# Optimization experiments

Measured on AMD Instinct MI355X. Metric: run time of the kernel, lower is better.

The kernel has to match this reference:

```python
import jax, jax.numpy as jnp
import numpy as np

N_NODES = 50000
N_EDGES = 800000
IN_F = 128
HID = 64
H1 = 4  # heads layer 1
H2 = 1  # heads layer 2
N_GRAPHS = 32
NEG_SLOPE = 0.2  # PyG GATConv default leaky_relu slope


def _glorot(key, shape):
    fan_in, fan_out = shape[0], shape[-1]
    scale = jnp.sqrt(6.0 / (fan_in + fan_out))
    return jax.random.uniform(key, shape, jnp.float32, -scale, scale)


def setup_inputs() -> dict:
    key = jax.random.key(0)
    ks = jax.random.split(key, 10)
    x = jax.random.normal(ks[0], (N_NODES, IN_F), jnp.float32)
    edge_index = jax.random.randint(ks[1], (2, N_EDGES), 0, N_NODES, jnp.int64)
    batch = jnp.sort(jax.random.randint(ks[2], (N_NODES,), 0, N_GRAPHS, jnp.int64))
    # GATConv layer 1: in 128 -> 4 heads x 64, concat
    W1 = _glorot(ks[3], (IN_F, H1 * HID))
    a_src1 = _glorot(ks[4], (H1, HID))
    a_dst1 = _glorot(ks[5], (H1, HID))
    b1 = jnp.zeros((H1 * HID,), jnp.float32)
    # GATConv layer 2: in 256 -> 1 head x 64
    W2 = _glorot(ks[6], (H1 * HID, H2 * HID))
    a_src2 = _glorot(ks[7], (H2, HID))
    a_dst2 = _glorot(ks[8], (H2, HID))
    b2 = jnp.zeros((H2 * HID,), jnp.float32)
    return {"x": x, "edge_index": edge_index, "batch": batch,
            "W1": W1, "a_src1": a_src1, "a_dst1": a_dst1, "b1": b1,
            "W2": W2, "a_src2": a_src2, "a_dst2": a_dst2, "b2": b2}


def gat_layer(x, src, dst, W, a_src, a_dst, bias, num_nodes):
    """PyG-style GATConv with concat=True output [N, H*C]."""
    H, C = a_src.shape
    h = (x @ W).reshape(num_nodes, H, C)            # [N,H,C]
    alpha_src = jnp.sum(h * a_src[None], axis=-1)   # [N,H]
    alpha_dst = jnp.sum(h * a_dst[None], axis=-1)   # [N,H]
    e = jax.nn.leaky_relu(alpha_src[src] + alpha_dst[dst], NEG_SLOPE)  # [E,H]
    # segment softmax over destination neighborhoods
    m = jax.ops.segment_max(e, dst, num_segments=num_nodes)
    ex = jnp.exp(e - m[dst])
    denom = jax.ops.segment_sum(ex, dst, num_segments=num_nodes)
    alpha = ex / (denom[dst] + 1e-16)               # [E,H]
    out = jax.ops.segment_sum(h[src] * alpha[:, :, None], dst, num_segments=num_nodes)
    return out.reshape(num_nodes, H * C) + bias


def reference(x, edge_index, batch, W1, a_src1, a_dst1, b1, W2, a_src2, a_dst2, b2):
    N = x.shape[0]
    # PyG GATConv adds self-loops by default
    loops = jnp.arange(N, dtype=edge_index.dtype)
    src = jnp.concatenate([edge_index[0], loops])
    dst = jnp.concatenate([edge_index[1], loops])
    h = jax.nn.relu(gat_layer(x, src, dst, W1, a_src1, a_dst1, b1, N))
    h = gat_layer(h, src, dst, W2, a_src2, a_dst2, b2, N)
    # role == 'global': global mean pool over batch ids
    sums = jax.ops.segment_sum(h, batch, num_segments=N_GRAPHS)
    cnt = jax.ops.segment_sum(jnp.ones((N, 1), h.dtype), batch, num_segments=N_GRAPHS)
    return sums / jnp.maximum(cnt, 1.0)
```

## Files before the change

### kernel.cpp

```cpp
#include <hip/hip_runtime.h>
#include <cmath>

#define HID 64
typedef unsigned short ushort_t;
typedef __attribute__((ext_vector_type(8))) short bf16x8;
typedef __attribute__((ext_vector_type(4))) float f32x4;

__device__ inline ushort_t f2b(float f) {
    unsigned u = __float_as_uint(f);
    unsigned r = (u + 0x7fffu + ((u >> 16) & 1u)) >> 16;
    return (ushort_t)r;
}
__device__ inline float b2f(ushort_t b) { return __uint_as_float(((unsigned)b) << 16); }


__global__ void fill_i32(int* __restrict__ p, int v, long n) {
    long i = (long)blockIdx.x * blockDim.x + threadIdx.x;
    long stride = (long)gridDim.x * blockDim.x;
    for (; i < n; i += stride) p[i] = v;
}

__global__ __launch_bounds__(256) void prep_k(const float* __restrict__ W1,
                                              const float* __restrict__ W2,
                                              ushort_t* __restrict__ W1t,
                                              ushort_t* __restrict__ W2t,
                                              const int* __restrict__ batch,
                                              int* __restrict__ cnt_i,
                                              float* __restrict__ outp,
                                              int N, int NHB) {
    int b = blockIdx.x;
    int t = threadIdx.x;
    if (b < 128) {
        W1t[(size_t)t * 128 + b] = f2b(W1[(size_t)b * 256 + t]);
    } else if (b < 384) {
        int k = b - 128;
        if (t < 64) W2t[(size_t)t * 256 + k] = f2b(W2[(size_t)k * 64 + t]);
    } else if (b < 384 + NHB) {
        __shared__ int lh[32];
        if (t < 32) lh[t] = 0;
        __syncthreads();
        int i = (b - 384) * 256 + t;
        if (i < N) atomicAdd(&lh[batch[i]], 1);
        __syncthreads();
        if (t < 32 && lh[t] > 0) atomicAdd(&cnt_i[t], lh[t]);
    } else {
        int i = t * 8;
        #pragma unroll
        for (int j = 0; j < 8; ++j) outp[i + j] = 0.f;
    }
}

template<int WM, int WN, int K, bool AF32, bool B_WHOLE, int AH>
__global__ __launch_bounds__(WM * WN * 64) void gemm_mfma(
        const void* __restrict__ Ap, const ushort_t* __restrict__ Bt,
        ushort_t* __restrict__ Cb, const float* __restrict__ a_src,
        const float* __restrict__ a_dst, float* __restrict__ os,
        float* __restrict__ od, int M) {
    constexpr int T = WM * WN * 64;
    constexpr int BM = WM * 64;
    constexpr int BN = WN * 64;
    constexpr int BSTR = B_WHOLE ? (K + 8) : 40;

    __shared__ ushort_t Alds[BM][40];
    __shared__ ushort_t Blds[BN][BSTR];

    const int tid = threadIdx.x;
    const int bm = blockIdx.x * BM;
    const int w = tid >> 6;
    const int l = tid & 63;
    const int lr = l >> 4;
    const int lc = l & 15;
    const int row0 = (WM == 1) ? 0 : w * 64;
    const int col0 = (WN == 1) ? 0 : w * 64;

    f32x4 acc[4][4] = {};

    if (B_WHOLE) {
        constexpr int UPR = K / 8;
        for (int u = tid; u < BN * UPR; u += T) {
            int row = u / UPR, j = u % UPR;
            *(bf16x8*)&Blds[row][j * 8] = *(const bf16x8*)&Bt[(size_t)row * K + j * 8];
        }
    }

    for (int kk = 0; kk < K / 32; ++kk) {
        __syncthreads();
        for (int u = tid; u < BM * 4; u += T) {
            int row = u >> 2, part = u & 3;
            int gm = bm + row;
            bf16x8 v = {0, 0, 0, 0, 0, 0, 0, 0};
            if (gm < M) {
                if (AF32) {
                    const float* ap = (const float*)Ap + (size_t)gm * K + kk * 32 + part * 8;
                    float4 v0 = *(const float4*)ap;
                    float4 v1 = *(const float4*)(ap + 4);
                    v[0] = (short)f2b(v0.x); v[1] = (short)f2b(v0.y);
                    v[2] = (short)f2b(v0.z); v[3] = (short)f2b(v0.w);
                    v[4] = (short)f2b(v1.x); v[5] = (short)f2b(v1.y);
                    v[6] = (short)f2b(v1.z); v[7] = (short)f2b(v1.w);
                } else {
                    v = *(const bf16x8*)((const ushort_t*)Ap + (size_t)gm * K + kk * 32 + part * 8);
                }
            }
            *(bf16x8*)&Alds[row][part * 8] = v;
        }
        if (!B_WHOLE) {
            for (int u = tid; u < BN * 4; u += T) {
                int col = u >> 2, part = u & 3;
                *(bf16x8*)&Blds[col][part * 8] =
                    *(const bf16x8*)&Bt[(size_t)col * K + kk * 32 + part * 8];
            }
        }
        __syncthreads();

        const int koff = B_WHOLE ? kk * 32 : 0;
        bf16x8 af[4], bfr[4];
        #pragma unroll
        for (int fr = 0; fr < 4; ++fr)
            af[fr] = *(const bf16x8*)&Alds[row0 + fr * 16 + lc][lr * 8];
        #pragma unroll
        for (int fc = 0; fc < 4; ++fc)
            bfr[fc] = *(const bf16x8*)&Blds[col0 + fc * 16 + lc][koff + lr * 8];
        #pragma unroll
        for (int fr = 0; fr < 4; ++fr)
            #pragma unroll
            for (int fc = 0; fc < 4; ++fc)
                acc[fr][fc] = __builtin_amdgcn_mfma_f32_16x16x32_bf16(
                    af[fr], bfr[fc], acc[fr][fc], 0, 0, 0);
    }

    #pragma unroll
    for (int fr = 0; fr < 4; ++fr)
        #pragma unroll
        for (int r = 0; r < 4; ++r) {
            int gm = bm + row0 + fr * 16 + lr * 4 + r;
            if (gm >= M) continue;
            #pragma unroll
            for (int fc = 0; fc < 4; ++fc)
                Cb[(size_t)gm * BN + col0 + fc * 16 + lc] = f2b(acc[fr][fc][r]);
        }

    if (AH > 0) {
        const int head = (WN > 1) ? w : 0;
        const float* __restrict__ asv = a_src + head * 64;
        const float* __restrict__ adv = a_dst + head * 64;
        #pragma unroll
        for (int fr = 0; fr < 4; ++fr)
            #pragma unroll
            for (int r = 0; r < 4; ++r) {
                float ps = 0.f, pd = 0.f;
                #pragma unroll
                for (int fc = 0; fc < 4; ++fc) {
                    float av = acc[fr][fc][r];
                    ps = fmaf(av, asv[fc * 16 + lc], ps);
                    pd = fmaf(av, adv[fc * 16 + lc], pd);
                }
                #pragma unroll
                for (int off = 1; off < 16; off <<= 1) {
                    ps += __shfl_xor(ps, off, 64);
                    pd += __shfl_xor(pd, off, 64);
                }
                int gm = bm + row0 + fr * 16 + lr * 4 + r;
                if (lc == 0 && gm < M) {
                    os[(size_t)gm * AH + head] = ps;
                    od[(size_t)gm * AH + head] = pd;
                }
            }
    }
}


__global__ void count_k(const int* __restrict__ ei, int E, int N, int* __restrict__ deg) {
    int e = blockIdx.x * blockDim.x + threadIdx.x;
    int T = E + N;
    if (e >= T) return;
    int d = (e < E) ? ei[E + e] : (e - E);
    atomicAdd(&deg[d], 1);
}

__global__ __launch_bounds__(256) void scan1_k(const int* __restrict__ deg,
                                               int* __restrict__ bsum, int N) {
    int i = blockIdx.x * 256 + threadIdx.x;
    int v = (i < N) ? deg[i] : 0;
    #pragma unroll
    for (int off = 32; off > 0; off >>= 1) v += __shfl_xor(v, off, 64);
    __shared__ int ws[4];
    if ((threadIdx.x & 63) == 0) ws[threadIdx.x >> 6] = v;
    __syncthreads();
    if (threadIdx.x == 0) bsum[blockIdx.x] = ws[0] + ws[1] + ws[2] + ws[3];
}

__global__ __launch_bounds__(256) void scan3_k(const int* __restrict__ deg,
                                               const int* __restrict__ bsum,
                                               int* __restrict__ rowstart, int N, int NB) {
    int t = threadIdx.x;
    int lane = t & 63, wave = t >> 6;
    int pv = (t < NB && t < (int)blockIdx.x) ? bsum[t] : 0;
    #pragma unroll
    for (int off = 32; off > 0; off >>= 1) pv += __shfl_xor(pv, off, 64);
    __shared__ int wsp[4];
    if (lane == 0) wsp[wave] = pv;
    __syncthreads();
    int base = wsp[0] + wsp[1] + wsp[2] + wsp[3];

    int i = blockIdx.x * 256 + t;
    int v = (i < N) ? deg[i] : 0;
    int inc = v;
    #pragma unroll
    for (int off = 1; off < 64; off <<= 1) {
        int u = __shfl_up(inc, off, 64);
        if (lane >= off) inc += u;
    }
    __shared__ int wsum[4];
    if (lane == 63) wsum[wave] = inc;
    __syncthreads();
    int woff = base;
    for (int w = 0; w < wave; ++w) woff += wsum[w];
    int excl = inc - v + woff;
    if (i < N) rowstart[i] = excl;
    if (i == N - 1) rowstart[N] = excl + v;
}

__global__ void scatter_k(const int* __restrict__ ei, int E, int N,
                          const int* __restrict__ rowstart, int* __restrict__ cursor,
                          int* __restrict__ srcs) {
    int e = blockIdx.x * blockDim.x + threadIdx.x;
    int T = E + N;
    if (e >= T) return;
    int s, d;
    if (e < E) { s = ei[e]; d = ei[E + e]; } else { s = e - E; d = s; }
    int p = atomicAdd(&cursor[d], 1);
    srcs[rowstart[d] + p] = s;
}

#define MAXD 128
__global__ __launch_bounds__(256) void gat_agg4(const ushort_t* __restrict__ hb,
        const int* __restrict__ rowstart, const int* __restrict__ srcs,
        const float* __restrict__ as, const float* __restrict__ ad,
        const float* __restrict__ bias, ushort_t* __restrict__ outb, int N) {
    __shared__ int ssrc_s[4][MAXD];
    __shared__ float sw_s[4][MAXD][4];
    __shared__ float hstat_s[4][2][4];
    const int wave = threadIdx.x >> 6;
    const int lane = threadIdx.x & 63;
    int d = blockIdx.x * 4 + wave;
    if (d >= N) return;
    int* ssrc = ssrc_s[wave];
    float (*sw)[4] = sw_s[wave];
    int beg = rowstart[d];
    int deg = rowstart[d + 1] - beg;
    int dcap = deg < MAXD ? deg : MAXD;
    for (int i = lane; i < dcap; i += 64) ssrc[i] = srcs[beg + i];

    const int isub = lane >> 2;
    const int hd = lane & 3;
    float adv = ad[d * 4 + hd];
    float vmax = -INFINITY;
    for (int e0 = 0; e0 < deg; e0 += 16) {
        int e = e0 + isub;
        if (e < deg) {
            int s = (e < MAXD) ? ssrc[e] : srcs[beg + e];
            float v = as[s * 4 + hd] + adv;
            v = v > 0.f ? v : 0.2f * v;
            if (e < MAXD) sw[e][hd] = v;
            vmax = fmaxf(vmax, v);
        }
    }
    #pragma unroll
    for (int off = 4; off < 64; off <<= 1) vmax = fmaxf(vmax, __shfl_xor(vmax, off, 64));
    float dsum = 0.f;
    for (int e0 = 0; e0 < deg; e0 += 16) {
        int e = e0 + isub;
        if (e < deg) {
            float v;
            if (e < MAXD) v = sw[e][hd];
            else {
                int s = srcs[beg + e];
                v = as[s * 4 + hd] + adv;
                v = v > 0.f ? v : 0.2f * v;
            }
            float ex = __expf(v - vmax);
            if (e < MAXD) sw[e][hd] = ex;
            dsum += ex;
        }
    }
    #pragma unroll
    for (int off = 4; off < 64; off <<= 1) dsum += __shfl_xor(dsum, off, 64);
    float rden = 1.f / (dsum + 1e-16f);
    for (int e0 = 0; e0 < dcap; e0 += 16) {
        int e = e0 + isub;
        if (e < dcap) sw[e][hd] *= rden;
    }
    if (deg > MAXD && isub == 0) {
        hstat_s[wave][0][hd] = vmax;
        hstat_s[wave][1][hd] = rden;
    }

    const int hd2 = lane >> 4;
    const ushort_t* __restrict__ hrow = hb + (size_t)(lane * 4);
    float a0 = 0.f, a1 = 0.f, a2 = 0.f, a3 = 0.f;
    int e = 0;
    for (; e + 4 <= dcap; e += 4) {
        int s0 = __builtin_amdgcn_readfirstlane(ssrc[e]);
        int s1 = __builtin_amdgcn_readfirstlane(ssrc[e + 1]);
        int s2 = __builtin_amdgcn_readfirstlane(ssrc[e + 2]);
        int s3 = __builtin_amdgcn_readfirstlane(ssrc[e + 3]);
        ushort4 g0 = *(const ushort4*)(hrow + (size_t)s0 * 256);
        ushort4 g1 = *(const ushort4*)(hrow + (size_t)s1 * 256);
        ushort4 g2 = *(const ushort4*)(hrow + (size_t)s2 * 256);
        ushort4 g3 = *(const ushort4*)(hrow + (size_t)s3 * 256);
        float w0 = sw[e][hd2], w1 = sw[e + 1][hd2];
        float w2 = sw[e + 2][hd2], w3 = sw[e + 3][hd2];
        a0 = fmaf(b2f(g0.x), w0, a0); a1 = fmaf(b2f(g0.y), w0, a1);
        a2 = fmaf(b2f(g0.z), w0, a2); a3 = fmaf(b2f(g0.w), w0, a3);
        a0 = fmaf(b2f(g1.x), w1, a0); a1 = fmaf(b2f(g1.y), w1, a1);
        a2 = fmaf(b2f(g1.z), w1, a2); a3 = fmaf(b2f(g1.w), w1, a3);
        a0 = fmaf(b2f(g2.x), w2, a0); a1 = fmaf(b2f(g2.y), w2, a1);
        a2 = fmaf(b2f(g2.z), w2, a2); a3 = fmaf(b2f(g2.w), w2, a3);
        a0 = fmaf(b2f(g3.x), w3, a0); a1 = fmaf(b2f(g3.y), w3, a1);
        a2 = fmaf(b2f(g3.z), w3, a2); a3 = fmaf(b2f(g3.w), w3, a3);
    }
    for (; e < dcap; ++e) {
        int s = __builtin_amdgcn_readfirstlane(ssrc[e]);
        float w = sw[e][hd2];
        ushort4 g = *(const ushort4*)(hrow + (size_t)s * 256);
        a0 = fmaf(b2f(g.x), w, a0); a1 = fmaf(b2f(g.y), w, a1);
        a2 = fmaf(b2f(g.z), w, a2); a3 = fmaf(b2f(g.w), w, a3);
    }
    if (deg > MAXD) {
        float vm2 = hstat_s[wave][0][hd2];
        float rd2 = hstat_s[wave][1][hd2];
        float adv2 = ad[d * 4 + hd2];
        for (int j = MAXD; j < deg; ++j) {
            int s = srcs[beg + j];
            float v = as[s * 4 + hd2] + adv2;
            v = v > 0.f ? v : 0.2f * v;
            float w = __expf(v - vm2) * rd2;
            ushort4 g = *(const ushort4*)(hrow + (size_t)s * 256);
            a0 = fmaf(b2f(g.x), w, a0); a1 = fmaf(b2f(g.y), w, a1);
            a2 = fmaf(b2f(g.z), w, a2); a3 = fmaf(b2f(g.w), w, a3);
        }
    }
    int cb = lane * 4;
    ushort4 ov;
    ov.x = f2b(fmaxf(a0 + bias[cb + 0], 0.f));
    ov.y = f2b(fmaxf(a1 + bias[cb + 1], 0.f));
    ov.z = f2b(fmaxf(a2 + bias[cb + 2], 0.f));
    ov.w = f2b(fmaxf(a3 + bias[cb + 3], 0.f));
    *(ushort4*)&outb[(size_t)d * 256 + cb] = ov;
}

__global__ __launch_bounds__(256) void gat_agg1(const ushort_t* __restrict__ hb,
        const int* __restrict__ rowstart, const int* __restrict__ srcs,
        const float* __restrict__ as, const float* __restrict__ ad,
        const float* __restrict__ bias, const int* __restrict__ batch,
        const int* __restrict__ cnt_i, float* __restrict__ outp, int N) {
    __shared__ int ssrc_s[4][MAXD];
    __shared__ float sw_s[4][MAXD];
    __shared__ float prow[4][64];
    __shared__ int gws[4];
    const int wave = threadIdx.x >> 6;
    const int lane = threadIdx.x & 63;
    int d = blockIdx.x * 4 + wave;
    bool active = d < N;
    if (active) {
        int* ssrc = ssrc_s[wave];
        float* sw = sw_s[wave];
        int beg = rowstart[d];
        int deg = rowstart[d + 1] - beg;
        int dcap = deg < MAXD ? deg : MAXD;
        for (int i = lane; i < dcap; i += 64) ssrc[i] = srcs[beg + i];

        float adv = ad[d];
        float vmax = -INFINITY;
        for (int e0 = 0; e0 < deg; e0 += 64) {
            int e = e0 + lane;
            if (e < deg) {
                int s = (e < MAXD) ? ssrc[e] : srcs[beg + e];
                float v = as[s] + adv;
                v = v > 0.f ? v : 0.2f * v;
                if (e < MAXD) sw[e] = v;
                vmax = fmaxf(vmax, v);
            }
        }
        #pragma unroll
        for (int off = 1; off < 64; off <<= 1) vmax = fmaxf(vmax, __shfl_xor(vmax, off, 64));
        float dsum = 0.f;
        for (int e0 = 0; e0 < deg; e0 += 64) {
            int e = e0 + lane;
            if (e < deg) {
                float v;
                if (e < MAXD) v = sw[e];
                else {
                    int s = srcs[beg + e];
                    v = as[s] + adv;
                    v = v > 0.f ? v : 0.2f * v;
                }
                float ex = __expf(v - vmax);
                if (e < MAXD) sw[e] = ex;
                dsum += ex;
            }
        }
        #pragma unroll
        for (int off = 1; off < 64; off <<= 1) dsum += __shfl_xor(dsum, off, 64);
        float rden = 1.f / (dsum + 1e-16f);
        for (int e0 = 0; e0 < dcap; e0 += 64) {
            int e = e0 + lane;
            if (e < dcap) sw[e] *= rden;
        }

        const int esub = lane >> 4;
        const int cg = lane & 15;
        const ushort_t* __restrict__ hrow = hb + (size_t)(cg * 4);
        float a0 = 0.f, a1 = 0.f, a2 = 0.f, a3 = 0.f;
        int e0 = 0;
        for (; e0 + 4 <= dcap; e0 += 4) {
            int e = e0 + esub;
            int s = ssrc[e];
            float w = sw[e];
            ushort4 g = *(const ushort4*)(hrow + (size_t)s * 64);
            a0 = fmaf(b2f(g.x), w, a0); a1 = fmaf(b2f(g.y), w, a1);
            a2 = fmaf(b2f(g.z), w, a2); a3 = fmaf(b2f(g.w), w, a3);
        }
        if (e0 < dcap) {
            int e = e0 + esub;
            if (e < dcap) {
                int s = ssrc[e];
                float w = sw[e];
                ushort4 g = *(const ushort4*)(hrow + (size_t)s * 64);
                a0 = fmaf(b2f(g.x), w, a0); a1 = fmaf(b2f(g.y), w, a1);
                a2 = fmaf(b2f(g.z), w, a2); a3 = fmaf(b2f(g.w), w, a3);
            }
        }
        for (int j = MAXD + esub; j < deg; j += 4) {
            int s = srcs[beg + j];
            float v = as[s] + adv;
            v = v > 0.f ? v : 0.2f * v;
            float w = __expf(v - vmax) * rden;
            ushort4 g = *(const ushort4*)(hrow + (size_t)s * 64);
            a0 = fmaf(b2f(g.x), w, a0); a1 = fmaf(b2f(g.y), w, a1);
            a2 = fmaf(b2f(g.z), w, a2); a3 = fmaf(b2f(g.w), w, a3);
        }
        a0 += __shfl_xor(a0, 16, 64); a0 += __shfl_xor(a0, 32, 64);
        a1 += __shfl_xor(a1, 16, 64); a1 += __shfl_xor(a1, 32, 64);
        a2 += __shfl_xor(a2, 16, 64); a2 += __shfl_xor(a2, 32, 64);
        a3 += __shfl_xor(a3, 16, 64); a3 += __shfl_xor(a3, 32, 64);
        int g = batch[d];
        if (esub == 0) {
            float cntf = fmaxf((float)cnt_i[g], 1.f);
            float rc = 1.f / cntf;
            int cb = cg * 4;
            float4 o;
            o.x = (a0 + bias[cb + 0]) * rc;
            o.y = (a1 + bias[cb + 1]) * rc;
            o.z = (a2 + bias[cb + 2]) * rc;
            o.w = (a3 + bias[cb + 3]) * rc;
            *(float4*)&prow[wave][cb] = o;
        }
        if (lane == 0) gws[wave] = g;
    } else {
        if (lane == 0) gws[wave] = -1;
    }
    __syncthreads();
    if (threadIdx.x < 64) {
        int t = threadIdx.x;
        int g0 = gws[0];
        if (g0 >= 0 && gws[1] == g0 && gws[2] == g0 && gws[3] == g0) {
            atomicAdd(&outp[g0 * 64 + t],
                      prow[0][t] + prow[1][t] + prow[2][t] + prow[3][t]);
        } else {
            #pragma unroll
            for (int w2 = 0; w2 < 4; ++w2)
                if (gws[w2] >= 0) atomicAdd(&outp[gws[w2] * 64 + t], prow[w2][t]);
        }
    }
}


extern "C" void kernel_launch(void* const* d_in, const int* in_sizes, int n_in,
                              void* d_out, int out_size, void* d_ws, size_t ws_size,
                              hipStream_t stream) {
    const float* x      = (const float*)d_in[0];
    const int*   ei     = (const int*)d_in[1];
    const int*   batch  = (const int*)d_in[2];
    const float* W1     = (const float*)d_in[3];
    const float* a_src1 = (const float*)d_in[4];
    const float* a_dst1 = (const float*)d_in[5];
    const float* b1     = (const float*)d_in[6];
    const float* W2     = (const float*)d_in[7];
    const float* a_src2 = (const float*)d_in[8];
    const float* a_dst2 = (const float*)d_in[9];
    const float* b2     = (const float*)d_in[10];
    float* out = (float*)d_out;

    const int N = in_sizes[0] / 128;
    const int E = in_sizes[1] / 2;
    const int F1 = 256;
    const int F2 = 64;
    const int T = E + N;
    const int NB = (N + 255) / 256;

    float* ws = (float*)d_ws;
    size_t o = 0;
    ushort_t* h1b   = (ushort_t*)(ws + o); o += (size_t)N * F1 / 2;
    ushort_t* out1b = (ushort_t*)(ws + o); o += (size_t)N * F1 / 2;
    ushort_t* h2b   = (ushort_t*)(ws + o); o += (size_t)N * F2 / 2;
    float* asrc1 = ws + o; o += (size_t)N * 4;
    float* adst1 = ws + o; o += (size_t)N * 4;
    float* asrc2 = ws + o; o += (size_t)N;
    float* adst2 = ws + o; o += (size_t)N;
    ushort_t* W1t = (ushort_t*)(ws + o); o += 256 * 128 / 2;
    ushort_t* W2t = (ushort_t*)(ws + o); o += 64 * 256 / 2;
    int* ib = (int*)(ws + o);
    size_t io = 0;
    int* deg      = ib + io; io += N;
    int* cursor   = ib + io; io += N;
    int* cnt_i    = ib + io; io += 32;
    int* rowstart = ib + io; io += N + 1;
    int* bsum     = ib + io; io += NB;
    int* srcs     = ib + io; io += T;
    (void)ws_size; (void)n_in; (void)out_size;

    fill_i32<<<256, 256, 0, stream>>>(deg, 0, 2L * N + 32);
    prep_k<<<384 + NB + 1, 256, 0, stream>>>(W1, W2, W1t, W2t, batch, cnt_i, out, N, NB);

    count_k<<<(T + 255) / 256, 256, 0, stream>>>(ei, E, N, deg);
    scan1_k<<<NB, 256, 0, stream>>>(deg, bsum, N);
    scan3_k<<<NB, 256, 0, stream>>>(deg, bsum, rowstart, N, NB);
    scatter_k<<<(T + 255) / 256, 256, 0, stream>>>(ei, E, N, rowstart, cursor, srcs);

    gemm_mfma<1, 4, 128, true, false, 4><<<(N + 63) / 64, 256, 0, stream>>>(
        x, W1t, h1b, a_src1, a_dst1, asrc1, adst1, N);
    gat_agg4<<<(N + 3) / 4, 256, 0, stream>>>(h1b, rowstart, srcs, asrc1, adst1, b1, out1b, N);

    gemm_mfma<2, 1, 256, false, true, 1><<<(N + 127) / 128, 128, 0, stream>>>(
        out1b, W2t, h2b, a_src2, a_dst2, asrc2, adst2, N);
    gat_agg1<<<(N + 3) / 4, 256, 0, stream>>>(h2b, rowstart, srcs, asrc2, adst2, b2,
                                              batch, cnt_i, out, N);
}
```

Measured before the change: 256.1 us.

## Merge degree count into prep and CSR scatter into layer-1 GEMM launch

Degree counting moves into the prep kernel as extra blocks, and the CSR scatter runs as extra blocks of a new fused kernel that also does the layer-1 GEMM. Both changes cut kernel launches and let independent work share a grid. The aggregation inner loop is also unrolled by two so two gathers are in flight at once. The cost is a larger combined kernel with mixed block types, and more register pressure in the aggregation loop.

Measured after the change: 237.7 us, median of 3. 7.2% less time.

```diff
diff --git a/kernel.cpp b/kernel.cpp
--- a/kernel.cpp
+++ b/kernel.cpp
@@ -27,7 +27,9 @@
                                               const int* __restrict__ batch,
                                               int* __restrict__ cnt_i,
                                               float* __restrict__ outp,
-                                              int N, int NHB) {
+                                              const int* __restrict__ ei,
+                                              int* __restrict__ deg,
+                                              int N, int E, int NHB) {
     int b = blockIdx.x;
     int t = threadIdx.x;
     if (b < 128) {
@@ -35,24 +37,189 @@
     } else if (b < 384) {
         int k = b - 128;
         if (t < 64) W2t[(size_t)t * 256 + k] = f2b(W2[(size_t)k * 64 + t]);
-    } else if (b < 384 + NHB) {
+    } else if (b == 384) {
+        int i = t * 8;
+        #pragma unroll
+        for (int j = 0; j < 8; ++j) outp[i + j] = 0.f;
+    } else if (b < 385 + NHB) {
         __shared__ int lh[32];
         if (t < 32) lh[t] = 0;
         __syncthreads();
-        int i = (b - 384) * 256 + t;
+        int i = (b - 385) * 256 + t;
         if (i < N) atomicAdd(&lh[batch[i]], 1);
         __syncthreads();
         if (t < 32 && lh[t] > 0) atomicAdd(&cnt_i[t], lh[t]);
     } else {
-        int i = t * 8;
-        #pragma unroll
-        for (int j = 0; j < 8; ++j) outp[i + j] = 0.f;
-    }
-}
-
-template<int WM, int WN, int K, bool AF32, bool B_WHOLE, int AH>
+        int e = (b - 385 - NHB) * 256 + t;
+        int T = E + N;
+        if (e < T) {
+            int d = (e < E) ? ei[E + e] : (e - E);
+            atomicAdd(&deg[d], 1);
+        }
+    }
+}
+
+
+__global__ __launch_bounds__(256) void scan1_k(const int* __restrict__ deg,
+                                               int* __restrict__ bsum, int N) {
+    int i = blockIdx.x * 256 + threadIdx.x;
+    int v = (i < N) ? deg[i] : 0;
+    #pragma unroll
+    for (int off = 32; off > 0; off >>= 1) v += __shfl_xor(v, off, 64);
+    __shared__ int ws[4];
+    if ((threadIdx.x & 63) == 0) ws[threadIdx.x >> 6] = v;
+    __syncthreads();
+    if (threadIdx.x == 0) bsum[blockIdx.x] = ws[0] + ws[1] + ws[2] + ws[3];
+}
+
+__global__ __launch_bounds__(256) void scan3_k(const int* __restrict__ deg,
+                                               const int* __restrict__ bsum,
+                                               int* __restrict__ rowstart, int N, int NB) {
+    int t = threadIdx.x;
+    int lane = t & 63, wave = t >> 6;
+    int pv = (t < NB && t < (int)blockIdx.x) ? bsum[t] : 0;
+    #pragma unroll
+    for (int off = 32; off > 0; off >>= 1) pv += __shfl_xor(pv, off, 64);
+    __shared__ int wsp[4];
+    if (lane == 0) wsp[wave] = pv;
+    __syncthreads();
+    int base = wsp[0] + wsp[1] + wsp[2] + wsp[3];
+
+    int i = blockIdx.x * 256 + t;
+    int v = (i < N) ? deg[i] : 0;
+    int inc = v;
+    #pragma unroll
+    for (int off = 1; off < 64; off <<= 1) {
+        int u = __shfl_up(inc, off, 64);
+        if (lane >= off) inc += u;
+    }
+    __shared__ int wsum[4];
+    if (lane == 63) wsum[wave] = inc;
+    __syncthreads();
+    int woff = base;
+    for (int w = 0; w < wave; ++w) woff += wsum[w];
+    int excl = inc - v + woff;
+    if (i < N) rowstart[i] = excl;
+    if (i == N - 1) rowstart[N] = excl + v;
+}
+
+__global__ __launch_bounds__(256) void mega1_k(
+        const float* __restrict__ x, const ushort_t* __restrict__ Bt,
+        ushort_t* __restrict__ Cb, const float* __restrict__ a_src,
+        const float* __restrict__ a_dst, float* __restrict__ os,
+        float* __restrict__ od, int M, int NG1,
+        const int* __restrict__ ei, int E, int N,
+        const int* __restrict__ rowstart, int* __restrict__ cursor,
+        int* __restrict__ srcs) {
+    __shared__ ushort_t Alds[64][40];
+    __shared__ ushort_t Blds[256][40];
+    const int tid = threadIdx.x;
+
+    if (blockIdx.x >= NG1) {
+        int e = (blockIdx.x - NG1) * 256 + tid;
+        int T = E + N;
+        if (e < T) {
+            int s, d;
+            if (e < E) { s = ei[e]; d = ei[E + e]; } else { s = e - E; d = s; }
+            int p = atomicAdd(&cursor[d], 1);
+            srcs[rowstart[d] + p] = s;
+        }
+        return;
+    }
+
+    const int bm = blockIdx.x * 64;
+    const int w = tid >> 6;
+    const int l = tid & 63;
+    const int lr = l >> 4;
+    const int lc = l & 15;
+    const int col0 = w * 64;
+
+    f32x4 acc[4][4] = {};
+
+    for (int kk = 0; kk < 4; ++kk) {
+        __syncthreads();
+        {
+            int row = tid >> 2, part = tid & 3;
+            int gm = bm + row;
+            bf16x8 v = {0, 0, 0, 0, 0, 0, 0, 0};
+            if (gm < M) {
+                const float* ap = x + (size_t)gm * 128 + kk * 32 + part * 8;
+                float4 v0 = *(const float4*)ap;
+                float4 v1 = *(const float4*)(ap + 4);
+                v[0] = (short)f2b(v0.x); v[1] = (short)f2b(v0.y);
+                v[2] = (short)f2b(v0.z); v[3] = (short)f2b(v0.w);
+                v[4] = (short)f2b(v1.x); v[5] = (short)f2b(v1.y);
+                v[6] = (short)f2b(v1.z); v[7] = (short)f2b(v1.w);
+            }
+            *(bf16x8*)&Alds[row][part * 8] = v;
+        }
+        #pragma unroll
+        for (int it = 0; it < 4; ++it) {
+            int u = tid + it * 256;
+            int col = u >> 2, part = u & 3;
+            *(bf16x8*)&Blds[col][part * 8] =
+                *(const bf16x8*)&Bt[(size_t)col * 128 + kk * 32 + part * 8];
+        }
+        __syncthreads();
+
+        bf16x8 af[4], bfr[4];
+        #pragma unroll
+        for (int fr = 0; fr < 4; ++fr)
+            af[fr] = *(const bf16x8*)&Alds[fr * 16 + lc][lr * 8];
+        #pragma unroll
+        for (int fc = 0; fc < 4; ++fc)
+            bfr[fc] = *(const bf16x8*)&Blds[col0 + fc * 16 + lc][lr * 8];
+        #pragma unroll
+        for (int fr = 0; fr < 4; ++fr)
+            #pragma unroll
+            for (int fc = 0; fc < 4; ++fc)
+                acc[fr][fc] = __builtin_amdgcn_mfma_f32_16x16x32_bf16(
+                    af[fr], bfr[fc], acc[fr][fc], 0, 0, 0);
+    }
+
+    #pragma unroll
+    for (int fr = 0; fr < 4; ++fr)
+        #pragma unroll
+        for (int r = 0; r < 4; ++r) {
+            int gm = bm + fr * 16 + lr * 4 + r;
+            if (gm >= M) continue;
+            #pragma unroll
+            for (int fc = 0; fc < 4; ++fc)
+                Cb[(size_t)gm * 256 + col0 + fc * 16 + lc] = f2b(acc[fr][fc][r]);
+        }
+
+    {
+        const int head = w;
+        const float* __restrict__ asv = a_src + head * 64;
+        const float* __restrict__ adv = a_dst + head * 64;
+        #pragma unroll
+        for (int fr = 0; fr < 4; ++fr)
+            #pragma unroll
+            for (int r = 0; r < 4; ++r) {
+                float ps = 0.f, pd = 0.f;
+                #pragma unroll
+                for (int fc = 0; fc < 4; ++fc) {
+                    float av = acc[fr][fc][r];
+                    ps = fmaf(av, asv[fc * 16 + lc], ps);
+                    pd = fmaf(av, adv[fc * 16 + lc], pd);
+                }
+                #pragma unroll
+                for (int off = 1; off < 16; off <<= 1) {
+                    ps += __shfl_xor(ps, off, 64);
+                    pd += __shfl_xor(pd, off, 64);
+                }
+                int gm = bm + fr * 16 + lr * 4 + r;
+                if (lc == 0 && gm < M) {
+                    os[(size_t)gm * 4 + head] = ps;
+                    od[(size_t)gm * 4 + head] = pd;
+                }
+            }
+    }
+}
+
+template<int WM, int WN, int K, bool B_WHOLE, int AH>
 __global__ __launch_bounds__(WM * WN * 64) void gemm_mfma(
-        const void* __restrict__ Ap, const ushort_t* __restrict__ Bt,
+        const ushort_t* __restrict__ Ap, const ushort_t* __restrict__ Bt,
         ushort_t* __restrict__ Cb, const float* __restrict__ a_src,
         const float* __restrict__ a_dst, float* __restrict__ os,
         float* __restrict__ od, int M) {
@@ -89,19 +256,8 @@
             int row = u >> 2, part = u & 3;
             int gm = bm + row;
             bf16x8 v = {0, 0, 0, 0, 0, 0, 0, 0};
-            if (gm < M) {
-                if (AF32) {
-                    const float* ap = (const float*)Ap + (size_t)gm * K + kk * 32 + part * 8;
-                    float4 v0 = *(const float4*)ap;
-                    float4 v1 = *(const float4*)(ap + 4);
-                    v[0] = (short)f2b(v0.x); v[1] = (short)f2b(v0.y);
-                    v[2] = (short)f2b(v0.z); v[3] = (short)f2b(v0.w);
-                    v[4] = (short)f2b(v1.x); v[5] = (short)f2b(v1.y);
-                    v[6] = (short)f2b(v1.z); v[7] = (short)f2b(v1.w);
-                } else {
-                    v = *(const bf16x8*)((const ushort_t*)Ap + (size_t)gm * K + kk * 32 + part * 8);
-                }
-            }
+            if (gm < M)
+                v = *(const bf16x8*)(Ap + (size_t)gm * K + kk * 32 + part * 8);
             *(bf16x8*)&Alds[row][part * 8] = v;
         }
         if (!B_WHOLE) {
@@ -167,70 +323,6 @@
                 }
             }
     }
-}
-
-
-__global__ void count_k(const int* __restrict__ ei, int E, int N, int* __restrict__ deg) {
-    int e = blockIdx.x * blockDim.x + threadIdx.x;
-    int T = E + N;
-    if (e >= T) return;
-    int d = (e < E) ? ei[E + e] : (e - E);
-    atomicAdd(&deg[d], 1);
-}
-
-__global__ __launch_bounds__(256) void scan1_k(const int* __restrict__ deg,
-                                               int* __restrict__ bsum, int N) {
-    int i = blockIdx.x * 256 + threadIdx.x;
-    int v = (i < N) ? deg[i] : 0;
-    #pragma unroll
-    for (int off = 32; off > 0; off >>= 1) v += __shfl_xor(v, off, 64);
-    __shared__ int ws[4];
-    if ((threadIdx.x & 63) == 0) ws[threadIdx.x >> 6] = v;
-    __syncthreads();
-    if (threadIdx.x == 0) bsum[blockIdx.x] = ws[0] + ws[1] + ws[2] + ws[3];
-}
-
-__global__ __launch_bounds__(256) void scan3_k(const int* __restrict__ deg,
-                                               const int* __restrict__ bsum,
-                                               int* __restrict__ rowstart, int N, int NB) {
-    int t = threadIdx.x;
-    int lane = t & 63, wave = t >> 6;
-    int pv = (t < NB && t < (int)blockIdx.x) ? bsum[t] : 0;
-    #pragma unroll
-    for (int off = 32; off > 0; off >>= 1) pv += __shfl_xor(pv, off, 64);
-    __shared__ int wsp[4];
-    if (lane == 0) wsp[wave] = pv;
-    __syncthreads();
-    int base = wsp[0] + wsp[1] + wsp[2] + wsp[3];
-
-    int i = blockIdx.x * 256 + t;
-    int v = (i < N) ? deg[i] : 0;
-    int inc = v;
-    #pragma unroll
-    for (int off = 1; off < 64; off <<= 1) {
-        int u = __shfl_up(inc, off, 64);
-        if (lane >= off) inc += u;
-    }
-    __shared__ int wsum[4];
-    if (lane == 63) wsum[wave] = inc;
-    __syncthreads();
-    int woff = base;
-    for (int w = 0; w < wave; ++w) woff += wsum[w];
-    int excl = inc - v + woff;
-    if (i < N) rowstart[i] = excl;
-    if (i == N - 1) rowstart[N] = excl + v;
-}
-
-__global__ void scatter_k(const int* __restrict__ ei, int E, int N,
-                          const int* __restrict__ rowstart, int* __restrict__ cursor,
-                          int* __restrict__ srcs) {
-    int e = blockIdx.x * blockDim.x + threadIdx.x;
-    int T = E + N;
-    if (e >= T) return;
-    int s, d;
-    if (e < E) { s = ei[e]; d = ei[E + e]; } else { s = e - E; d = s; }
-    int p = atomicAdd(&cursor[d], 1);
-    srcs[rowstart[d] + p] = s;
 }
 
 #define MAXD 128
@@ -414,15 +506,18 @@
         const ushort_t* __restrict__ hrow = hb + (size_t)(cg * 4);
         float a0 = 0.f, a1 = 0.f, a2 = 0.f, a3 = 0.f;
         int e0 = 0;
-        for (; e0 + 4 <= dcap; e0 += 4) {
-            int e = e0 + esub;
-            int s = ssrc[e];
-            float w = sw[e];
-            ushort4 g = *(const ushort4*)(hrow + (size_t)s * 64);
-            a0 = fmaf(b2f(g.x), w, a0); a1 = fmaf(b2f(g.y), w, a1);
-            a2 = fmaf(b2f(g.z), w, a2); a3 = fmaf(b2f(g.w), w, a3);
-        }
-        if (e0 < dcap) {
+        for (; e0 + 8 <= dcap; e0 += 8) {
+            int eA = e0 + esub, eB = e0 + esub + 4;
+            int sA = ssrc[eA], sB = ssrc[eB];
+            float wA = sw[eA], wB = sw[eB];
+            ushort4 gA = *(const ushort4*)(hrow + (size_t)sA * 64);
+            ushort4 gB = *(const ushort4*)(hrow + (size_t)sB * 64);
+            a0 = fmaf(b2f(gA.x), wA, a0); a1 = fmaf(b2f(gA.y), wA, a1);
+            a2 = fmaf(b2f(gA.z), wA, a2); a3 = fmaf(b2f(gA.w), wA, a3);
+            a0 = fmaf(b2f(gB.x), wB, a0); a1 = fmaf(b2f(gB.y), wB, a1);
+            a2 = fmaf(b2f(gB.z), wB, a2); a3 = fmaf(b2f(gB.w), wB, a3);
+        }
+        for (; e0 < dcap; e0 += 4) {
             int e = e0 + esub;
             if (e < dcap) {
                 int s = ssrc[e];
@@ -499,6 +594,8 @@
     const int F2 = 64;
     const int T = E + N;
     const int NB = (N + 255) / 256;
+    const int NCB = (T + 255) / 256;
+    const int NG1 = (N + 63) / 64;
 
     float* ws = (float*)d_ws;
     size_t o = 0;
@@ -522,18 +619,19 @@
     (void)ws_size; (void)n_in; (void)out_size;
 
     fill_i32<<<256, 256, 0, stream>>>(deg, 0, 2L * N + 32);
-    prep_k<<<384 + NB + 1, 256, 0, stream>>>(W1, W2, W1t, W2t, batch, cnt_i, out, N, NB);
-
-    count_k<<<(T + 255) / 256, 256, 0, stream>>>(ei, E, N, deg);
+    prep_k<<<385 + NB + NCB, 256, 0, stream>>>(W1, W2, W1t, W2t, batch, cnt_i, out,
+                                               ei, deg, N, E, NB);
+
     scan1_k<<<NB, 256, 0, stream>>>(deg, bsum, N);
     scan3_k<<<NB, 256, 0, stream>>>(deg, bsum, rowstart, N, NB);
-    scatter_k<<<(T + 255) / 256, 256, 0, stream>>>(ei, E, N, rowstart, cursor, srcs);
-
-    gemm_mfma<1, 4, 128, true, false, 4><<<(N + 63) / 64, 256, 0, stream>>>(
-        x, W1t, h1b, a_src1, a_dst1, asrc1, adst1, N);
+
+    mega1_k<<<NG1 + NCB, 256, 0, stream>>>(x, W1t, h1b, a_src1, a_dst1,
+                                           asrc1, adst1, N, NG1,
+                                           ei, E, N, rowstart, cursor, srcs);
+
     gat_agg4<<<(N + 3) / 4, 256, 0, stream>>>(h1b, rowstart, srcs, asrc1, adst1, b1, out1b, N);
 
-    gemm_mfma<2, 1, 256, false, true, 1><<<(N + 127) / 128, 128, 0, stream>>>(
+    gemm_mfma<2, 1, 256, true, 1><<<(N + 127) / 128, 128, 0, stream>>>(
         out1b, W2t, h2b, a_src2, a_dst2, asrc2, adst2, N);
     gat_agg1<<<(N + 3) / 4, 256, 0, stream>>>(h2b, rowstart, srcs, asrc2, adst2, b2,
                                               batch, cnt_i, out, N);
```
